# Performance work log

Hardware: AMD Instinct MI355X
Metric: run time of the kernel (lower is better)

The kernel has to match this reference:

```python
import jax, jax.numpy as jnp
import numpy as np

DIM = 512
HEADS = 8
DIM_HEAD = 64
INNER = HEADS * DIM_HEAD  # 512
BN_EPS = 1e-5


def _bn(x, gamma, beta, mean, var):
    # BatchNorm1d in eval mode over channel axis 1 of [b, c, n]
    inv = gamma / jnp.sqrt(var + BN_EPS)
    return x * inv[None, :, None] + (beta - mean * inv)[None, :, None]


def setup_inputs() -> dict:
    key = jax.random.key(0)
    ks = jax.random.split(key, 12)
    b, d, n = 4, DIM, 2048
    s = 0.02
    return {
        "x": jax.random.normal(ks[0], (b, d, n), dtype=jnp.float32),
        "W_qkv": jax.random.normal(ks[1], (3 * INNER, DIM), dtype=jnp.float32) * s,
        "W_out": jax.random.normal(ks[2], (DIM, INNER), dtype=jnp.float32) * s,
        "b_out": jax.random.normal(ks[3], (DIM,), dtype=jnp.float32) * s,
        "g1": jax.random.normal(ks[4], (DIM,), dtype=jnp.float32) * 0.1 + 1.0,
        "beta1": jax.random.normal(ks[5], (DIM,), dtype=jnp.float32) * 0.1,
        "m1": jax.random.normal(ks[6], (DIM,), dtype=jnp.float32) * 0.1,
        "v1": jax.random.uniform(ks[7], (DIM,), minval=0.5, maxval=1.5, dtype=jnp.float32),
        "W_ffn": jax.random.normal(ks[8], (DIM, DIM), dtype=jnp.float32) * s,
        "g2": jax.random.normal(ks[9], (DIM,), dtype=jnp.float32) * 0.1 + 1.0,
        "beta2": jax.random.normal(ks[10], (DIM,), dtype=jnp.float32) * 0.1,
        "m2": jax.random.normal(ks[11], (DIM,), dtype=jnp.float32) * 0.1,
        "v2": jax.random.uniform(jax.random.fold_in(key, 99), (DIM,), minval=0.5, maxval=1.5, dtype=jnp.float32),
    }


def reference(x, W_qkv, W_out, b_out, g1, beta1, m1, v1, W_ffn, g2, beta2, m2, v2):
    b, d, n = x.shape
    h, dh = HEADS, DIM_HEAD
    scale = dh ** -0.5

    # ---- Attention (manual QKV + einsum softmax attention) ----
    xt = jnp.einsum("bdn->bnd", x)                       # [b, n, d]
    qkv = xt @ W_qkv.T                                   # [b, n, 3*inner]
    q, k, v = jnp.split(qkv, 3, axis=-1)
    def to_heads(t):
        return t.reshape(b, n, h, dh).transpose(0, 2, 1, 3)  # [b, h, n, dh]
    q, k, v = to_heads(q), to_heads(k), to_heads(v)
    dots = jnp.einsum("bhid,bhjd->bhij", q, k) * scale   # [b, h, n, n]
    attn = jax.nn.softmax(dots, axis=-1)
    out = jnp.einsum("bhij,bhjd->bhid", attn, v)         # [b, h, n, dh]
    out = out.transpose(0, 2, 1, 3).reshape(b, n, h * dh).transpose(0, 2, 1)  # [b, inner, n]
    # to_out: Conv1d(inner, dim, 1, bias=True) + BatchNorm1d(dim)
    out = jnp.einsum("oc,bcn->bon", W_out, out) + b_out[None, :, None]
    att_out = _bn(out, g1, beta1, m1, v1)

    # ---- Residual + GELU, then FFN (Conv1d 1x1 no bias + BN), residual + GELU ----
    att = jax.nn.gelu(att_out + x, approximate=False)
    ffn = _bn(jnp.einsum("oc,bcn->bon", W_ffn, att), g2, beta2, m2, v2)
    return jax.nn.gelu(att + ffn, approximate=False)
```

## Files before the change

kernel.cpp:

```cpp
#include <hip/hip_runtime.h>
#include <math.h>

#define N_TOK 2048

typedef __attribute__((ext_vector_type(8))) short short8;
typedef __attribute__((ext_vector_type(4))) float f32x4;
typedef __attribute__((ext_vector_type(16))) float f32x16;

__device__ __forceinline__ float gelu_f(float v) {
    return 0.5f * v * (1.0f + erff(v * 0.7071067811865475f));
}
__device__ __forceinline__ ushort f2bf(float x) {
    uint u = __float_as_uint(x);
    uint r = u + 0x7FFFu + ((u >> 16) & 1u);
    return (ushort)(r >> 16);
}
__device__ __forceinline__ float bf2f(ushort u) {
    return __uint_as_float((uint)u << 16);
}
__device__ __forceinline__ void gload16(const void* g, void* s) {
    __builtin_amdgcn_global_load_lds((const __attribute__((address_space(1))) void*)g,
                                     (__attribute__((address_space(3))) void*)s, 16, 0, 0);
}

__global__ __launch_bounds__(256)
void prep(const float* __restrict__ w0, ushort* __restrict__ o0,
          const float* __restrict__ w1, ushort* __restrict__ o1,
          const float* __restrict__ w2, ushort* __restrict__ o2,
          const float* __restrict__ x, ushort* __restrict__ xt)
{
    __shared__ ushort sT[64 * 68];
    const int tid = threadIdx.x;
    int bx = blockIdx.x;
    if (bx < 1280) {
        int i4 = bx * 256 + tid;
        const float* src; ushort* dst; int idx;
        if (i4 < 196608)      { src = w0; dst = o0; idx = i4; }
        else if (i4 < 262144) { src = w1; dst = o1; idx = i4 - 196608; }
        else                  { src = w2; dst = o2; idx = i4 - 262144; }
        float4 v = *(const float4*)&src[idx * 4];
        ushort4 p; p.x = f2bf(v.x); p.y = f2bf(v.y); p.z = f2bf(v.z); p.w = f2bf(v.w);
        *(ushort4*)&dst[idx * 4] = p;
        return;
    }
    bx -= 1280;
    const int tok0 = (bx & 31) * 64;
    const int ch0 = ((bx >> 5) & 7) * 64;
    const int bi = bx >> 8;
    #pragma unroll
    for (int i = 0; i < 4; i++) {
        int ch = (tid >> 4) + i * 16;
        int t4 = (tid & 15) * 4;
        float4 v = *(const float4*)&x[((size_t)bi * 512 + ch0 + ch) * N_TOK + tok0 + t4];
        ushort4 p; p.x = f2bf(v.x); p.y = f2bf(v.y); p.z = f2bf(v.z); p.w = f2bf(v.w);
        *(ushort4*)&sT[ch * 68 + t4] = p;
    }
    __syncthreads();
    const int tr = (tid & 15) + (tid >> 6) * 16;
    const int cb = ((tid >> 4) & 3) * 16;
    uint vv[8];
    #pragma unroll
    for (int j = 0; j < 8; j++) {
        uint lo = sT[(cb + 2 * j) * 68 + tr];
        uint hi = sT[(cb + 2 * j + 1) * 68 + tr];
        vv[j] = lo | (hi << 16);
    }
    size_t base = ((size_t)bi * N_TOK + tok0 + tr) * 512 + ch0 + cb;
    *(uint4*)&xt[base]     = *(uint4*)&vv[0];
    *(uint4*)&xt[base + 8] = *(uint4*)&vv[4];
}

template<int MODE, int BM, int BN>
__global__ __launch_bounds__(256)
void bgemm(const ushort* __restrict__ A, const ushort* __restrict__ Bt, int M,
           ushort* __restrict__ qt, ushort* __restrict__ vc,
           float* __restrict__ outF, ushort* __restrict__ outB,
           const float* __restrict__ bias,
           const float* __restrict__ g, const float* __restrict__ be,
           const float* __restrict__ mu, const float* __restrict__ va,
           const ushort* __restrict__ residB)
{
    constexpr int MF = BM / 32, NF = BN / 32;
    __shared__ ushort sA[BM * 64];
    __shared__ ushort sB[BN * 64];
    const int tid = threadIdx.x;
    const int w = tid >> 6, l = tid & 63;
    const int l16 = l & 15, lg = l >> 4;
    const int wr = w >> 1, wc = w & 1;
    const int bi = blockIdx.z;
    const int m0 = blockIdx.y * BM, n0 = blockIdx.x * BN;
    const ushort* Bb = Bt + (size_t)bi * N_TOK * 512;
    const int srow = l >> 3, spos = l & 7;

    f32x4 acc[MF][NF];
    #pragma unroll
    for (int i = 0; i < MF; i++)
        #pragma unroll
        for (int j = 0; j < NF; j++) acc[i][j] = (f32x4){0.f, 0.f, 0.f, 0.f};

    for (int kt = 0; kt < 512; kt += 64) {
        __syncthreads();
        #pragma unroll
        for (int i = 0; i < BM / 32; i++) {
            int row = w * (BM / 4) + i * 8 + srow;
            int c = spos ^ (row & 7);
            gload16(A + (size_t)(m0 + row) * 512 + kt + c * 8,
                    sA + (w * (BM / 4) + i * 8) * 64);
        }
        #pragma unroll
        for (int i = 0; i < BN / 32; i++) {
            int row = w * (BN / 4) + i * 8 + srow;
            int c = spos ^ (row & 7);
            gload16(Bb + (size_t)(n0 + row) * 512 + kt + c * 8,
                    sB + (w * (BN / 4) + i * 8) * 64);
        }
        __syncthreads();
        #pragma unroll
        for (int ks = 0; ks < 2; ks++) {
            short8 af[MF], bfv[NF];
            #pragma unroll
            for (int mi = 0; mi < MF; mi++) {
                int row = wr * (BM / 2) + mi * 16 + l16;
                af[mi] = *(const short8*)&sA[row * 64 + (((ks * 4 + lg) ^ (row & 7)) << 3)];
            }
            #pragma unroll
            for (int ni = 0; ni < NF; ni++) {
                int row = wc * (BN / 2) + ni * 16 + l16;
                bfv[ni] = *(const short8*)&sB[row * 64 + (((ks * 4 + lg) ^ (row & 7)) << 3)];
            }
            __builtin_amdgcn_s_setprio(1);
            #pragma unroll
            for (int mi = 0; mi < MF; mi++)
                #pragma unroll
                for (int ni = 0; ni < NF; ni++)
                    acc[mi][ni] = __builtin_amdgcn_mfma_f32_16x16x32_bf16(
                        af[mi], bfv[ni], acc[mi][ni], 0, 0, 0);
            __builtin_amdgcn_s_setprio(0);
        }
    }

    const int chb = m0 + wr * (BM / 2);
    const int tkb = n0 + wc * (BN / 2);
    if (MODE == 0) {
        if (m0 < 1024) {
            const float qs = (m0 < 512) ? 0.18033688f : 1.0f;
            #pragma unroll
            for (int mi = 0; mi < MF; mi++) {
                int ob = chb + mi * 16 + lg * 4;
                #pragma unroll
                for (int ni = 0; ni < NF; ni++) {
                    int tok = tkb + ni * 16 + l16;
                    ushort4 p;
                    p.x = f2bf(acc[mi][ni][0] * qs); p.y = f2bf(acc[mi][ni][1] * qs);
                    p.z = f2bf(acc[mi][ni][2] * qs); p.w = f2bf(acc[mi][ni][3] * qs);
                    *(ushort4*)&qt[((size_t)bi * N_TOK + tok) * 1024 + ob] = p;
                }
            }
        } else {
            #pragma unroll
            for (int mi = 0; mi < MF; mi++)
                #pragma unroll
                for (int r = 0; r < 4; r++) {
                    int o = chb + mi * 16 + lg * 4 + r - 1024;
                    #pragma unroll
                    for (int ni = 0; ni < NF; ni++) {
                        int tok = tkb + ni * 16 + l16;
                        vc[((size_t)bi * 512 + o) * N_TOK + tok] = f2bf(acc[mi][ni][r]);
                    }
                }
        }
    } else {
        #pragma unroll
        for (int mi = 0; mi < MF; mi++) {
            float inv[4], sh[4], bb[4];
            #pragma unroll
            for (int r = 0; r < 4; r++) {
                int o = chb + mi * 16 + lg * 4 + r;
                inv[r] = g[o] * rsqrtf(va[o] + 1e-5f);
                sh[r]  = be[o] - mu[o] * inv[r];
                bb[r]  = (MODE == 1) ? bias[o] : 0.f;
            }
            #pragma unroll
            for (int ni = 0; ni < NF; ni++) {
                int tok = tkb + ni * 16 + l16;
                ushort4 rv = *(const ushort4*)&residB[((size_t)bi * N_TOK + tok) * 512 +
                                                      chb + mi * 16 + lg * 4];
                float rr_[4] = {bf2f(rv.x), bf2f(rv.y), bf2f(rv.z), bf2f(rv.w)};
                float ov[4];
                #pragma unroll
                for (int r = 0; r < 4; r++) {
                    float y = (acc[mi][ni][r] + bb[r]) * inv[r] + sh[r];
                    ov[r] = gelu_f((MODE == 1) ? (y + rr_[r]) : (rr_[r] + y));
                }
                if (MODE == 1) {
                    ushort4 p;
                    p.x = f2bf(ov[0]); p.y = f2bf(ov[1]);
                    p.z = f2bf(ov[2]); p.w = f2bf(ov[3]);
                    *(ushort4*)&outB[((size_t)bi * N_TOK + tok) * 512 +
                                     chb + mi * 16 + lg * 4] = p;
                } else {
                    #pragma unroll
                    for (int r = 0; r < 4; r++) {
                        int o = chb + mi * 16 + lg * 4 + r;
                        outF[((size_t)bi * 512 + o) * N_TOK + tok] = ov[r];
                    }
                }
            }
        }
    }
}

__global__ __launch_bounds__(128)
void attn_mfma(const ushort* __restrict__ qt, const ushort* __restrict__ vc,
               ushort* __restrict__ aout)
{
    __shared__ ushort sK[2][64 * 64];
    __shared__ ushort sV[2][64 * 64];
    const int tid = threadIdx.x;
    const int w = tid >> 6, l = tid & 63;
    const int c = l & 31, h = l >> 5;
    const int phys = blockIdx.x;
    const int logi = (phys & 7) * 128 + (phys >> 3);
    const int qblk = logi & 31;
    const int pair = logi >> 5;
    const int hh = pair & 7, bi = pair >> 3;
    const int qw = qblk * 64 + w * 32;
    const int srow = l >> 3, spos = l & 7;

    const ushort* kSrc = qt + (size_t)bi * N_TOK * 1024 + 512 + hh * 64 + ((spos ^ srow) << 3);
    const ushort* vSrc = vc + (size_t)(bi * 512 + hh * 64) * N_TOK + ((spos ^ srow) << 3);

    short8 qf[4];
    #pragma unroll
    for (int dk = 0; dk < 4; dk++)
        qf[dk] = *(const short8*)(qt +
            (size_t)(bi * N_TOK + qw + c) * 1024 + hh * 64 + dk * 16 + h * 8);

    f32x16 oacc[2];
    #pragma unroll
    for (int dt = 0; dt < 2; dt++)
        #pragma unroll
        for (int i = 0; i < 16; i++) oacc[dt][i] = 0.f;
    float lsum = 0.f;

    #pragma unroll
    for (int i = 0; i < 4; i++) {
        int rb = i * 16 + w * 8;
        gload16(kSrc + (size_t)(rb + srow) * 1024, &sK[0][rb * 64]);
        gload16(vSrc + (size_t)(rb + srow) * N_TOK, &sV[0][rb * 64]);
    }

    for (int t = 0; t < N_TOK / 64; t++) {
        const int cur = t & 1;
        __syncthreads();
        if (t + 1 < N_TOK / 64) {
            const int kv1 = (t + 1) * 64;
            #pragma unroll
            for (int i = 0; i < 4; i++) {
                int rb = i * 16 + w * 8;
                gload16(kSrc + (size_t)(kv1 + rb + srow) * 1024,
                        &sK[cur ^ 1][rb * 64]);
                gload16(vSrc + (size_t)(rb + srow) * N_TOK + kv1,
                        &sV[cur ^ 1][rb * 64]);
            }
        }

        #pragma unroll
        for (int s = 0; s < 2; s++) {
            f32x16 sacc;
            #pragma unroll
            for (int i = 0; i < 16; i++) sacc[i] = 0.f;
            __builtin_amdgcn_s_setprio(1);
            #pragma unroll
            for (int dk = 0; dk < 4; dk++) {
                int row = s * 32 + c;
                short8 kf = *(const short8*)&sK[cur][row * 64 +
                             (((dk * 2 + h) ^ (row & 7)) << 3)];
                sacc = __builtin_amdgcn_mfma_f32_32x32x16_bf16(kf, qf[dk], sacc, 0, 0, 0);
            }
            __builtin_amdgcn_s_setprio(0);

            uint u0_0, u0_1, u1_0, u1_1, u2_0, u2_1, u3_0, u3_1;
            float ps = 0.f;
            {
                float p0, p1, p2, p3;
#define PACK_G(G, U0, U1) \
                p0 = __builtin_amdgcn_exp2f(sacc[4*G+0]); \
                p1 = __builtin_amdgcn_exp2f(sacc[4*G+1]); \
                p2 = __builtin_amdgcn_exp2f(sacc[4*G+2]); \
                p3 = __builtin_amdgcn_exp2f(sacc[4*G+3]); \
                ps += (p0 + p1) + (p2 + p3); \
                asm("v_cvt_pk_bf16_f32 %0, %1, %2" : "=v"(U0) : "v"(p0), "v"(p1)); \
                asm("v_cvt_pk_bf16_f32 %0, %1, %2" : "=v"(U1) : "v"(p2), "v"(p3));
                PACK_G(0, u0_0, u0_1)
                PACK_G(1, u1_0, u1_1)
                PACK_G(2, u2_0, u2_1)
                PACK_G(3, u3_0, u3_1)
#undef PACK_G
            }
            lsum += ps;

#define PV_STEP(T2, A0, A1, B0, B1) \
            { \
                uint a0 = A0, b0 = B0, a1 = A1, b1 = B1; \
                asm volatile("v_permlane32_swap_b32 %0, %1" : "+v"(b0), "+v"(a0)); \
                asm volatile("v_permlane32_swap_b32 %0, %1" : "+v"(b1), "+v"(a1)); \
                uint4 fu = make_uint4(a0, a1, b0, b1); \
                short8 pf = *(short8*)&fu; \
                __builtin_amdgcn_s_setprio(1); \
                _Pragma("unroll") \
                for (int dt = 0; dt < 2; dt++) { \
                    int row = dt * 32 + c; \
                    short8 vf = *(const short8*)&sV[cur][row * 64 + \
                                 (((s * 4 + T2 * 2 + h) ^ (row & 7)) << 3)]; \
                    oacc[dt] = __builtin_amdgcn_mfma_f32_32x32x16_bf16( \
                        pf, vf, oacc[dt], 0, 0, 0); \
                } \
                __builtin_amdgcn_s_setprio(0); \
            }
            PV_STEP(0, u0_0, u0_1, u1_0, u1_1)
            PV_STEP(1, u2_0, u2_1, u3_0, u3_1)
#undef PV_STEP
        }
    }

    lsum += __shfl_xor(lsum, 32);
    float rl = 1.f / lsum;
    #pragma unroll
    for (int dt = 0; dt < 2; dt++)
        #pragma unroll
        for (int g = 0; g < 4; g++) {
            float o0 = oacc[dt][4 * g + 0] * rl;
            float o1 = oacc[dt][4 * g + 1] * rl;
            float o2 = oacc[dt][4 * g + 2] * rl;
            float o3 = oacc[dt][4 * g + 3] * rl;
            uint p0, p1;
            asm("v_cvt_pk_bf16_f32 %0, %1, %2" : "=v"(p0) : "v"(o0), "v"(o1));
            asm("v_cvt_pk_bf16_f32 %0, %1, %2" : "=v"(p1) : "v"(o2), "v"(o3));
            int ch = hh * 64 + dt * 32 + 8 * g + 4 * h;
            *(uint2*)&aout[((size_t)bi * N_TOK + qw + c) * 512 + ch] = make_uint2(p0, p1);
        }
}

extern "C" void kernel_launch(void* const* d_in, const int* in_sizes, int n_in,
                              void* d_out, int out_size, void* d_ws, size_t ws_size,
                              hipStream_t stream) {
    const float* x    = (const float*)d_in[0];
    const float* Wqkv = (const float*)d_in[1];
    const float* Wout = (const float*)d_in[2];
    const float* bout = (const float*)d_in[3];
    const float* g1   = (const float*)d_in[4];
    const float* be1  = (const float*)d_in[5];
    const float* m1   = (const float*)d_in[6];
    const float* v1   = (const float*)d_in[7];
    const float* Wffn = (const float*)d_in[8];
    const float* g2   = (const float*)d_in[9];
    const float* be2  = (const float*)d_in[10];
    const float* m2   = (const float*)d_in[11];
    const float* v2   = (const float*)d_in[12];

    char* ws = (char*)d_ws;
    ushort* wqB  = (ushort*)(ws + 0);
    ushort* woB  = (ushort*)(ws + 1572864);
    ushort* wfB  = (ushort*)(ws + 2097152);
    ushort* xt   = (ushort*)(ws + 2621440);
    ushort* qtp  = (ushort*)(ws + 11010048);
    ushort* vcp  = (ushort*)(ws + 27787264);
    ushort* aout = (ushort*)(ws + 36175872);
    ushort* attB = (ushort*)(ws + 27787264);

    dim3 blk(256);
    prep<<<2304, blk, 0, stream>>>(Wqkv, wqB, Wout, woB, Wffn, wfB, x, xt);
    bgemm<0, 128, 128><<<dim3(16, 12, 4), blk, 0, stream>>>(
        wqB, xt, 1536, qtp, vcp, nullptr, nullptr,
        nullptr, nullptr, nullptr, nullptr, nullptr, nullptr);
    attn_mfma<<<dim3(1024), dim3(128), 0, stream>>>(qtp, vcp, aout);
    bgemm<1, 64, 128><<<dim3(16, 8, 4), blk, 0, stream>>>(
        woB, aout, 512, nullptr, nullptr, nullptr, attB,
        bout, g1, be1, m1, v1, xt);
    bgemm<2, 64, 128><<<dim3(16, 8, 4), blk, 0, stream>>>(
        wfB, attB, 512, nullptr, nullptr, (float*)d_out, nullptr,
        nullptr, g2, be2, m2, v2, attB);
}
```

Baseline: 123.0 us.

## Split attention over two KV halves and merge partial outputs in a separate kernel

```diff
diff --git a/kernel.cpp b/kernel.cpp
--- a/kernel.cpp
+++ b/kernel.cpp
@@ -78,7 +78,7 @@
            const float* __restrict__ bias,
            const float* __restrict__ g, const float* __restrict__ be,
            const float* __restrict__ mu, const float* __restrict__ va,
-           const ushort* __restrict__ residB)
+           const ushort* __restrict__ residB, const float* __restrict__ residF)
 {
     constexpr int MF = BM / 32, NF = BN / 32;
     __shared__ ushort sA[BM * 64];
@@ -183,9 +183,19 @@
             #pragma unroll
             for (int ni = 0; ni < NF; ni++) {
                 int tok = tkb + ni * 16 + l16;
-                ushort4 rv = *(const ushort4*)&residB[((size_t)bi * N_TOK + tok) * 512 +
-                                                      chb + mi * 16 + lg * 4];
-                float rr_[4] = {bf2f(rv.x), bf2f(rv.y), bf2f(rv.z), bf2f(rv.w)};
+                float rr_[4];
+                if (MODE == 1) {
+                    #pragma unroll
+                    for (int r = 0; r < 4; r++) {
+                        int o = chb + mi * 16 + lg * 4 + r;
+                        rr_[r] = residF[((size_t)bi * 512 + o) * N_TOK + tok];
+                    }
+                } else {
+                    ushort4 rv = *(const ushort4*)&residB[((size_t)bi * N_TOK + tok) * 512 +
+                                                          chb + mi * 16 + lg * 4];
+                    rr_[0] = bf2f(rv.x); rr_[1] = bf2f(rv.y);
+                    rr_[2] = bf2f(rv.z); rr_[3] = bf2f(rv.w);
+                }
                 float ov[4];
                 #pragma unroll
                 for (int r = 0; r < 4; r++) {
@@ -212,7 +222,8 @@
 
 __global__ __launch_bounds__(128)
 void attn_mfma(const ushort* __restrict__ qt, const ushort* __restrict__ vc,
-               ushort* __restrict__ aout)
+               ushort* __restrict__ oP0, ushort* __restrict__ oP1,
+               float* __restrict__ lP0, float* __restrict__ lP1)
 {
     __shared__ ushort sK[2][64 * 64];
     __shared__ ushort sV[2][64 * 64];
@@ -220,12 +231,17 @@
     const int w = tid >> 6, l = tid & 63;
     const int c = l & 31, h = l >> 5;
     const int phys = blockIdx.x;
-    const int logi = (phys & 7) * 128 + (phys >> 3);
-    const int qblk = logi & 31;
-    const int pair = logi >> 5;
+    const int logi = (phys & 7) * 256 + (phys >> 3);
+    const int kvh = logi & 1;
+    const int qblk = (logi >> 1) & 31;
+    const int pair = logi >> 6;
     const int hh = pair & 7, bi = pair >> 3;
     const int qw = qblk * 64 + w * 32;
     const int srow = l >> 3, spos = l & 7;
+    const int kvbase = kvh * 16;
+
+    ushort* oP = kvh ? oP1 : oP0;
+    float*  lP = kvh ? lP1 : lP0;
 
     const ushort* kSrc = qt + (size_t)bi * N_TOK * 1024 + 512 + hh * 64 + ((spos ^ srow) << 3);
     const ushort* vSrc = vc + (size_t)(bi * 512 + hh * 64) * N_TOK + ((spos ^ srow) << 3);
@@ -246,15 +262,15 @@
     #pragma unroll
     for (int i = 0; i < 4; i++) {
         int rb = i * 16 + w * 8;
-        gload16(kSrc + (size_t)(rb + srow) * 1024, &sK[0][rb * 64]);
-        gload16(vSrc + (size_t)(rb + srow) * N_TOK, &sV[0][rb * 64]);
-    }
-
-    for (int t = 0; t < N_TOK / 64; t++) {
+        gload16(kSrc + (size_t)(kvbase * 64 + rb + srow) * 1024, &sK[0][rb * 64]);
+        gload16(vSrc + (size_t)(rb + srow) * N_TOK + kvbase * 64, &sV[0][rb * 64]);
+    }
+
+    for (int t = 0; t < 16; t++) {
         const int cur = t & 1;
         __syncthreads();
-        if (t + 1 < N_TOK / 64) {
-            const int kv1 = (t + 1) * 64;
+        if (t + 1 < 16) {
+            const int kv1 = (kvbase + t + 1) * 64;
             #pragma unroll
             for (int i = 0; i < 4; i++) {
                 int rb = i * 16 + w * 8;
@@ -325,21 +341,51 @@
     }
 
     lsum += __shfl_xor(lsum, 32);
-    float rl = 1.f / lsum;
     #pragma unroll
     for (int dt = 0; dt < 2; dt++)
         #pragma unroll
         for (int g = 0; g < 4; g++) {
-            float o0 = oacc[dt][4 * g + 0] * rl;
-            float o1 = oacc[dt][4 * g + 1] * rl;
-            float o2 = oacc[dt][4 * g + 2] * rl;
-            float o3 = oacc[dt][4 * g + 3] * rl;
+            float o0 = oacc[dt][4 * g + 0];
+            float o1 = oacc[dt][4 * g + 1];
+            float o2 = oacc[dt][4 * g + 2];
+            float o3 = oacc[dt][4 * g + 3];
             uint p0, p1;
             asm("v_cvt_pk_bf16_f32 %0, %1, %2" : "=v"(p0) : "v"(o0), "v"(o1));
             asm("v_cvt_pk_bf16_f32 %0, %1, %2" : "=v"(p1) : "v"(o2), "v"(o3));
             int ch = hh * 64 + dt * 32 + 8 * g + 4 * h;
-            *(uint2*)&aout[((size_t)bi * N_TOK + qw + c) * 512 + ch] = make_uint2(p0, p1);
-        }
+            *(uint2*)&oP[((size_t)bi * N_TOK + qw + c) * 512 + ch] = make_uint2(p0, p1);
+        }
+    if (l < 32) lP[(size_t)(bi * 8 + hh) * N_TOK + qw + c] = lsum;
+}
+
+__global__ __launch_bounds__(256)
+void merge_o(const ushort* __restrict__ oP0, const ushort* __restrict__ oP1,
+             const float* __restrict__ lP0, const float* __restrict__ lP1,
+             ushort* __restrict__ aout)
+{
+    const int g16 = blockIdx.x * 256 + threadIdx.x;
+    const int trow = g16 >> 5;
+    const int ch0 = (g16 & 31) << 4;
+    const int bi = trow >> 11, tok = trow & 2047;
+    const int hh = ch0 >> 6;
+    const size_t li = (size_t)(bi * 8 + hh) * N_TOK + tok;
+    const float rl = 1.f / (lP0[li] + lP1[li]);
+    const size_t base = (size_t)trow * 512 + ch0;
+    uint4 a0 = *(const uint4*)&oP0[base];
+    uint4 b0 = *(const uint4*)&oP1[base];
+    uint4 a1 = *(const uint4*)&oP0[base + 8];
+    uint4 b1 = *(const uint4*)&oP1[base + 8];
+    uint o[8];
+    uint av[8] = {a0.x, a0.y, a0.z, a0.w, a1.x, a1.y, a1.z, a1.w};
+    uint bv[8] = {b0.x, b0.y, b0.z, b0.w, b1.x, b1.y, b1.z, b1.w};
+    #pragma unroll
+    for (int i = 0; i < 8; i++) {
+        float lo = (bf2f((ushort)(av[i] & 0xffff)) + bf2f((ushort)(bv[i] & 0xffff))) * rl;
+        float hi = (bf2f((ushort)(av[i] >> 16))    + bf2f((ushort)(bv[i] >> 16)))    * rl;
+        asm("v_cvt_pk_bf16_f32 %0, %1, %2" : "=v"(o[i]) : "v"(lo), "v"(hi));
+    }
+    *(uint4*)&aout[base]     = make_uint4(o[0], o[1], o[2], o[3]);
+    *(uint4*)&aout[base + 8] = make_uint4(o[4], o[5], o[6], o[7]);
 }
 
 extern "C" void kernel_launch(void* const* d_in, const int* in_sizes, int n_in,
@@ -361,24 +407,29 @@
 
     char* ws = (char*)d_ws;
     ushort* wqB  = (ushort*)(ws + 0);
+    float*  lP0  = (float*)(ws + 0);
+    float*  lP1  = (float*)(ws + 524288);
     ushort* woB  = (ushort*)(ws + 1572864);
     ushort* wfB  = (ushort*)(ws + 2097152);
     ushort* xt   = (ushort*)(ws + 2621440);
+    ushort* oP1  = (ushort*)(ws + 2621440);
     ushort* qtp  = (ushort*)(ws + 11010048);
+    ushort* aout = (ushort*)(ws + 11010048);
     ushort* vcp  = (ushort*)(ws + 27787264);
-    ushort* aout = (ushort*)(ws + 36175872);
     ushort* attB = (ushort*)(ws + 27787264);
+    ushort* oP0  = (ushort*)(ws + 36175872);
 
     dim3 blk(256);
     prep<<<2304, blk, 0, stream>>>(Wqkv, wqB, Wout, woB, Wffn, wfB, x, xt);
     bgemm<0, 128, 128><<<dim3(16, 12, 4), blk, 0, stream>>>(
         wqB, xt, 1536, qtp, vcp, nullptr, nullptr,
-        nullptr, nullptr, nullptr, nullptr, nullptr, nullptr);
-    attn_mfma<<<dim3(1024), dim3(128), 0, stream>>>(qtp, vcp, aout);
+        nullptr, nullptr, nullptr, nullptr, nullptr, nullptr, nullptr);
+    attn_mfma<<<dim3(2048), dim3(128), 0, stream>>>(qtp, vcp, oP0, oP1, lP0, lP1);
+    merge_o<<<dim3(1024), blk, 0, stream>>>(oP0, oP1, lP0, lP1, aout);
     bgemm<1, 64, 128><<<dim3(16, 8, 4), blk, 0, stream>>>(
         woB, aout, 512, nullptr, nullptr, nullptr, attB,
-        bout, g1, be1, m1, v1, xt);
+        bout, g1, be1, m1, v1, nullptr, x);
     bgemm<2, 64, 128><<<dim3(16, 8, 4), blk, 0, stream>>>(
         wfB, attB, 512, nullptr, nullptr, (float*)d_out, nullptr,
-        nullptr, g2, be2, m2, v2, attB);
-}
+        nullptr, g2, be2, m2, v2, attB, nullptr);
+}
```

Result: slower. 134.3 us (+9.2%).

## Use 4-wave attention blocks with triple-buffered K/V prefetch

Applied to the files above, without the earlier changes.

```diff
diff --git a/kernel.cpp b/kernel.cpp
--- a/kernel.cpp
+++ b/kernel.cpp
@@ -210,21 +210,21 @@
     }
 }
 
-__global__ __launch_bounds__(128)
+__global__ __launch_bounds__(256)
 void attn_mfma(const ushort* __restrict__ qt, const ushort* __restrict__ vc,
                ushort* __restrict__ aout)
 {
-    __shared__ ushort sK[2][64 * 64];
-    __shared__ ushort sV[2][64 * 64];
+    __shared__ ushort sK[3][64 * 64];
+    __shared__ ushort sV[3][64 * 64];
     const int tid = threadIdx.x;
     const int w = tid >> 6, l = tid & 63;
     const int c = l & 31, h = l >> 5;
     const int phys = blockIdx.x;
-    const int logi = (phys & 7) * 128 + (phys >> 3);
-    const int qblk = logi & 31;
-    const int pair = logi >> 5;
+    const int logi = (phys & 7) * 64 + (phys >> 3);
+    const int qblk = logi & 15;
+    const int pair = logi >> 4;
     const int hh = pair & 7, bi = pair >> 3;
-    const int qw = qblk * 64 + w * 32;
+    const int qw = qblk * 128 + w * 32;
     const int srow = l >> 3, spos = l & 7;
 
     const ushort* kSrc = qt + (size_t)bi * N_TOK * 1024 + 512 + hh * 64 + ((spos ^ srow) << 3);
@@ -243,27 +243,31 @@
         for (int i = 0; i < 16; i++) oacc[dt][i] = 0.f;
     float lsum = 0.f;
 
-    #pragma unroll
-    for (int i = 0; i < 4; i++) {
-        int rb = i * 16 + w * 8;
-        gload16(kSrc + (size_t)(rb + srow) * 1024, &sK[0][rb * 64]);
-        gload16(vSrc + (size_t)(rb + srow) * N_TOK, &sV[0][rb * 64]);
-    }
-
-    for (int t = 0; t < N_TOK / 64; t++) {
-        const int cur = t & 1;
-        __syncthreads();
-        if (t + 1 < N_TOK / 64) {
-            const int kv1 = (t + 1) * 64;
-            #pragma unroll
-            for (int i = 0; i < 4; i++) {
-                int rb = i * 16 + w * 8;
-                gload16(kSrc + (size_t)(kv1 + rb + srow) * 1024,
-                        &sK[cur ^ 1][rb * 64]);
-                gload16(vSrc + (size_t)(rb + srow) * N_TOK + kv1,
-                        &sV[cur ^ 1][rb * 64]);
-            }
-        }
+#define STAGE(T, BUF) \
+    { \
+        const int kv0_ = (T) * 64; \
+        _Pragma("unroll") \
+        for (int i_ = 0; i_ < 2; i_++) { \
+            int rb_ = w * 16 + i_ * 8; \
+            gload16(kSrc + (size_t)(kv0_ + rb_ + srow) * 1024, &sK[BUF][rb_ * 64]); \
+            gload16(vSrc + (size_t)(rb_ + srow) * N_TOK + kv0_, &sV[BUF][rb_ * 64]); \
+        } \
+    }
+
+    STAGE(0, 0)
+    STAGE(1, 1)
+
+    const int NT = N_TOK / 64;
+    for (int t = 0; t < NT; t++) {
+        if (t < NT - 1) { asm volatile("s_waitcnt vmcnt(4)" ::: "memory"); }
+        else            { asm volatile("s_waitcnt vmcnt(0)" ::: "memory"); }
+        __builtin_amdgcn_s_barrier();
+        __builtin_amdgcn_sched_barrier(0);
+        const int b_c = t % 3;
+        if (t + 2 < NT) { STAGE(t + 2, (t + 2) % 3) }
+
+        const ushort* kB = &sK[b_c][0];
+        const ushort* vB = &sV[b_c][0];
 
         #pragma unroll
         for (int s = 0; s < 2; s++) {
@@ -274,7 +278,7 @@
             #pragma unroll
             for (int dk = 0; dk < 4; dk++) {
                 int row = s * 32 + c;
-                short8 kf = *(const short8*)&sK[cur][row * 64 +
+                short8 kf = *(const short8*)&kB[row * 64 +
                              (((dk * 2 + h) ^ (row & 7)) << 3)];
                 sacc = __builtin_amdgcn_mfma_f32_32x32x16_bf16(kf, qf[dk], sacc, 0, 0, 0);
             }
@@ -311,7 +315,7 @@
                 _Pragma("unroll") \
                 for (int dt = 0; dt < 2; dt++) { \
                     int row = dt * 32 + c; \
-                    short8 vf = *(const short8*)&sV[cur][row * 64 + \
+                    short8 vf = *(const short8*)&vB[row * 64 + \
                                  (((s * 4 + T2 * 2 + h) ^ (row & 7)) << 3)]; \
                     oacc[dt] = __builtin_amdgcn_mfma_f32_32x32x16_bf16( \
                         pf, vf, oacc[dt], 0, 0, 0); \
@@ -323,6 +327,7 @@
 #undef PV_STEP
         }
     }
+#undef STAGE
 
     lsum += __shfl_xor(lsum, 32);
     float rl = 1.f / lsum;
@@ -374,7 +379,7 @@
     bgemm<0, 128, 128><<<dim3(16, 12, 4), blk, 0, stream>>>(
         wqB, xt, 1536, qtp, vcp, nullptr, nullptr,
         nullptr, nullptr, nullptr, nullptr, nullptr, nullptr);
-    attn_mfma<<<dim3(1024), dim3(128), 0, stream>>>(qtp, vcp, aout);
+    attn_mfma<<<dim3(512), dim3(256), 0, stream>>>(qtp, vcp, aout);
     bgemm<1, 64, 128><<<dim3(16, 8, 4), blk, 0, stream>>>(
         woB, aout, 512, nullptr, nullptr, nullptr, attB,
         bout, g1, be1, m1, v1, xt);
```

New measurement: 117.9 us. -4.2%, faster.
